# Performance work log

Measured on AMD Instinct MI355X. Metric: run time of the kernel, lower is better.

## Reference

```python
import jax, jax.numpy as jnp
import numpy as np

N = 100000
E = 3200000
D = 128


def setup_inputs() -> dict:
    key = jax.random.key(0)
    k1, k2, k3, k4 = jax.random.split(key, 4)
    x = jax.random.normal(k1, (N, D), dtype=jnp.float32)
    edge_index = jax.random.randint(k2, (2, E), 0, N, dtype=jnp.int64)
    W1 = jax.random.normal(k3, (D, 16), dtype=jnp.float32) * (1.0 / np.sqrt(D))
    b1 = jnp.zeros((16,), dtype=jnp.float32)
    W2 = jax.random.normal(k4, (16, 2), dtype=jnp.float32) * (1.0 / np.sqrt(16))
    b2 = jnp.zeros((2,), dtype=jnp.float32)
    return {"x": x, "edge_index": edge_index, "W1": W1, "b1": b1, "W2": W2, "b2": b2}


def _gcn_conv(h, src, dst, norm, W, b):
    # transform first (out_dim <= in_dim), then normalized scatter-add aggregation
    h = h @ W                                   # [N, out]
    msg = h[src] * norm[:, None]                # [E+N, out] gathered messages
    agg = jax.ops.segment_sum(msg, dst, num_segments=N)
    return agg + b


def reference(x, edge_index, W1, b1, W2, b2):
    loops = jnp.arange(N, dtype=edge_index.dtype)
    src = jnp.concatenate([edge_index[0], loops])   # row (message source)
    dst = jnp.concatenate([edge_index[1], loops])   # col (aggregation target)
    # symmetric GCN normalization: deg over dst, norm = d^-1/2[src] * d^-1/2[dst]
    deg = jax.ops.segment_sum(jnp.ones_like(src, dtype=x.dtype), dst, num_segments=N)
    dinv = jnp.where(deg > 0, jax.lax.rsqrt(deg), 0.0)
    norm = dinv[src] * dinv[dst]

    h = _gcn_conv(x, src, dst, norm, W1, b1)
    h = jax.nn.relu(h)
    h = _gcn_conv(h, src, dst, norm, W2, b2)
    return jax.nn.log_softmax(h, axis=1)
```

## Files before the change

### kernel.cpp

```cpp
#include <hip/hip_runtime.h>
#include <hip/hip_fp16.h>
#include <math.h>

#define N_NODES 100000
#define N_EDGES 3200000
#define D_IN    128
#define H1      16

#define BSH     8
#define NPB     256
#define NB      391
#define CAP     13056
#define PBLK    512
#define CHUNK   6250
#define ELS_CAP 12128
#define NLINES  (ELS_CAP / 16)
#define MROWS   64


__global__ __launch_bounds__(512) void k_zero(int* __restrict__ cursor) {
    int t = threadIdx.x;
    if (t < NB) cursor[t] = 0;
}

__global__ __launch_bounds__(512) void k_partition(const int* __restrict__ ei,
                                                   int* __restrict__ cursor,
                                                   unsigned int* __restrict__ eop) {
    __shared__ int h[512];
    __shared__ int loff[512];
    __shared__ int resv[NB];
    __shared__ unsigned short owner[NLINES];
    __shared__ unsigned char rank8[CHUNK];
    __shared__ unsigned int els[ELS_CAP];
    int t = threadIdx.x;
    h[t] = 0;
    __syncthreads();
    int c0 = blockIdx.x * CHUNK;
    const int* srcs = ei + c0;
    const int* dsts = ei + N_EDGES + c0;
    for (int i = t; i < CHUNK; i += 512)
        rank8[i] = (unsigned char)atomicAdd(&h[dsts[i] >> BSH], 1);
    __syncthreads();
    int cp = (h[t] + 15) & ~15;
    loff[t] = cp;
    __syncthreads();
    for (int o = 1; o < 512; o <<= 1) {
        int u = (t >= o) ? loff[t - o] : 0;
        __syncthreads();
        loff[t] += u;
        __syncthreads();
    }
    int inc = loff[t];
    int totalpad = loff[511];
    int ex = inc - cp;
    __syncthreads();
    loff[t] = ex;
    if (t < NB && cp) {
        resv[t] = atomicAdd(&cursor[t], cp);
        int l0 = ex >> 4;
        for (int k = 0; k < (cp >> 4); ++k) owner[l0 + k] = (unsigned short)t;
    }
    for (int i = t; i < totalpad; i += 512) els[i] = 0xFFFFFFFFu;
    __syncthreads();
    for (int i = t; i < CHUNK; i += 512) {
        int s = srcs[i];
        int d = dsts[i];
        int b = d >> BSH;
        els[loff[b] + (int)rank8[i]] = ((unsigned)s << BSH) | (unsigned)(d & (NPB - 1));
    }
    __syncthreads();
    for (int i = t; i < totalpad; i += 512) {
        int b   = owner[i >> 4];
        int pos = resv[b] + (i - loff[b]);
        if (pos < CAP)
            eop[(size_t)b * CAP + pos] = els[i];
    }
}

__global__ __launch_bounds__(512) void k_build(const int* __restrict__ cursor,
                                               unsigned int* __restrict__ eop,
                                               int* __restrict__ nstart,
                                               int* __restrict__ ndeg,
                                               float* __restrict__ dinv) {
    __shared__ unsigned int els[CAP];
    __shared__ int cnt[NPB];
    __shared__ int off[NPB];
    __shared__ int cur[NPB];
    int t = threadIdx.x, b = blockIdx.x;
    if (t < NPB) cnt[t] = 0;
    __syncthreads();
    int n = cursor[b]; if (n > CAP) n = CAP;
    unsigned int* reg = eop + (size_t)b * CAP;
    for (int i = t; i < n; i += 512) {
        unsigned int v = reg[i];
        els[i] = v;
        if ((int)v >= 0) atomicAdd(&cnt[v & (NPB - 1)], 1);
    }
    __syncthreads();
    int val = (t < NPB) ? cnt[t] : 0;
    if (t < NPB) off[t] = val;
    __syncthreads();
    for (int o = 1; o < NPB; o <<= 1) {
        int u = 0;
        if (t < NPB && t >= o) u = off[t - o];
        __syncthreads();
        if (t < NPB) off[t] += u;
        __syncthreads();
    }
    if (t < NPB) {
        int ex = off[t] - val;
        int node = (b << BSH) + t;
        if (node < N_NODES) {
            nstart[node] = b * CAP + ex;
            ndeg[node]   = val;
            dinv[node]   = rsqrtf((float)(val + 1));
        }
        cur[t] = ex;
    }
    __syncthreads();
    for (int i = t; i < n; i += 512) {
        unsigned int v = els[i];
        if ((int)v >= 0) {
            int r = atomicAdd(&cur[v & (NPB - 1)], 1);
            reg[r] = v >> BSH;
        }
    }
}

__global__ __launch_bounds__(256) void k_mm1(const float* __restrict__ x,
                                             const float* __restrict__ W1,
                                             const float* __restrict__ dinv,
                                             __half* __restrict__ h1h) {
    __shared__ float sX[MROWS][D_IN + 1];
    int t = threadIdx.x;
    int r0 = blockIdx.x * MROWS;
    for (int i = t; i < MROWS * (D_IN / 4); i += 256) {
        int row = i >> 5, c4 = i & 31;
        int grow = r0 + row;
        float4 v = (grow < N_NODES) ? ((const float4*)x)[(size_t)grow * 32 + c4]
                                    : make_float4(0.f, 0.f, 0.f, 0.f);
        sX[row][c4 * 4 + 0] = v.x; sX[row][c4 * 4 + 1] = v.y;
        sX[row][c4 * 4 + 2] = v.z; sX[row][c4 * 4 + 3] = v.w;
    }
    __syncthreads();
    int lane = t & 63;
    int c0 = __builtin_amdgcn_readfirstlane((t >> 6) * 4);
    float a0 = 0.f, a1 = 0.f, a2 = 0.f, a3 = 0.f;
#pragma unroll 4
    for (int d = 0; d < D_IN; ++d) {
        float xv = sX[lane][d];
        a0 = fmaf(xv, W1[d * 16 + c0 + 0], a0);
        a1 = fmaf(xv, W1[d * 16 + c0 + 1], a1);
        a2 = fmaf(xv, W1[d * 16 + c0 + 2], a2);
        a3 = fmaf(xv, W1[d * 16 + c0 + 3], a3);
    }
    int grow = r0 + lane;
    if (grow < N_NODES) {
        float di = dinv[grow];
        __half2* o = (__half2*)(h1h + (size_t)grow * H1 + c0);
        o[0] = __floats2half2_rn(a0 * di, a1 * di);
        o[1] = __floats2half2_rn(a2 * di, a3 * di);
    }
}

__global__ __launch_bounds__(256) void k_agg1(const unsigned int* __restrict__ eop,
                                              const int* __restrict__ nstart,
                                              const int* __restrict__ ndeg,
                                              const __half* __restrict__ h1h,
                                              const float* __restrict__ dinv,
                                              const float* __restrict__ b1,
                                              const float* __restrict__ W2,
                                              float2* __restrict__ h2f) {
    int t = threadIdx.x;
    int g = t >> 4, l = t & 15;
    int node = blockIdx.x * 16 + g;
    int e0 = nstart[node], e1 = e0 + ndeg[node];
    float acc = 0.f;
    int j = e0;
    for (; j + 4 <= e1; j += 4) {
        int s0 = eop[j], s1 = eop[j + 1], s2 = eop[j + 2], s3 = eop[j + 3];
        acc += __half2float(h1h[s0 * H1 + l]) + __half2float(h1h[s1 * H1 + l])
             + __half2float(h1h[s2 * H1 + l]) + __half2float(h1h[s3 * H1 + l]);
    }
    for (; j < e1; ++j) acc += __half2float(h1h[(int)eop[j] * H1 + l]);
    float di = dinv[node];
    float s  = acc + __half2float(h1h[node * H1 + l]);
    float h  = fmaxf(fmaf(di, s, b1[l]), 0.f);
    float p0 = h * W2[2 * l], p1 = h * W2[2 * l + 1];
#pragma unroll
    for (int off = 1; off < 16; off <<= 1) {
        p0 += __shfl_xor(p0, off);
        p1 += __shfl_xor(p1, off);
    }
    if (l == 0) h2f[node] = make_float2(p0 * di, p1 * di);
}

__global__ __launch_bounds__(256) void k_agg2(const unsigned int* __restrict__ eop,
                                              const int* __restrict__ nstart,
                                              const int* __restrict__ ndeg,
                                              const float2* __restrict__ h2f,
                                              const float* __restrict__ dinv,
                                              const float* __restrict__ b2,
                                              float* __restrict__ out) {
    int tg = blockIdx.x * 256 + threadIdx.x;
    int node = tg >> 2, l = tg & 3;
    if (node >= N_NODES) return;
    int e0 = nstart[node], e1 = e0 + ndeg[node];
    float ax = 0.f, ay = 0.f;
    for (int j = e0 + l; j < e1; j += 4) {
        float2 m = h2f[eop[j]];
        ax += m.x; ay += m.y;
    }
    ax += __shfl_xor(ax, 1); ay += __shfl_xor(ay, 1);
    ax += __shfl_xor(ax, 2); ay += __shfl_xor(ay, 2);
    if (l == 0) {
        float di = dinv[node];
        float2 self = h2f[node];
        float a0 = fmaf(di, ax + self.x, b2[0]);
        float a1 = fmaf(di, ay + self.y, b2[1]);
        float m  = fmaxf(a0, a1);
        float lg = logf(expf(a0 - m) + expf(a1 - m));
        out[2 * node]     = a0 - m - lg;
        out[2 * node + 1] = a1 - m - lg;
    }
}

extern "C" void kernel_launch(void* const* d_in, const int* in_sizes, int n_in,
                              void* d_out, int out_size, void* d_ws, size_t ws_size,
                              hipStream_t stream) {
    const float* x  = (const float*)d_in[0];
    const int*   ei = (const int*)d_in[1];
    const float* W1 = (const float*)d_in[2];
    const float* b1 = (const float*)d_in[3];
    const float* W2 = (const float*)d_in[4];
    const float* b2 = (const float*)d_in[5];
    float* out = (float*)d_out;

    int*          cursor = (int*)d_ws;
    int*          nstart = cursor + 512;
    int*          ndeg   = nstart + 100352;
    float*        dinv   = (float*)(ndeg + 100352);
    __half*       h1h    = (__half*)(dinv + 100352);
    float2*       h2f    = (float2*)(h1h + (size_t)100352 * H1);
    unsigned int* eop    = (unsigned int*)(h2f + 100352);

    k_zero     <<<1,    512, 0, stream>>>(cursor);
    k_partition<<<PBLK, 512, 0, stream>>>(ei, cursor, eop);
    k_build    <<<NB,   512, 0, stream>>>(cursor, eop, nstart, ndeg, dinv);
    k_mm1      <<<(N_NODES + MROWS - 1) / MROWS, 256, 0, stream>>>(x, W1, dinv, h1h);
    k_agg1     <<<N_NODES / 16, 256, 0, stream>>>(eop, nstart, ndeg, h1h, dinv, b1, W2, h2f);
    k_agg2     <<<(N_NODES * 4 + 255) / 256, 256, 0, stream>>>(eop, nstart, ndeg, h2f, dinv, b2, out);
}
```

Baseline: 222.0 us.

## Replace per-node CSR build with bucket-local shared-memory atomic aggregation

Drops the in-bucket counting sort that built per-node CSR offsets, keeping only a degree count. Both aggregation kernels now run one block per 256-node bucket, stream the unsorted packed edge list, and accumulate messages with shared-memory float atomics before the epilogue. This removes the prefix scan, the scatter rewrite of the edge array and the nstart/ndeg arrays. In exchange it adds LDS atomic contention, makes summation order nondeterministic, and limits aggregation to 391 blocks, which may lower occupancy.

```diff
diff --git a/kernel.cpp b/kernel.cpp
--- a/kernel.cpp
+++ b/kernel.cpp
@@ -77,53 +77,24 @@
     }
 }
 
-__global__ __launch_bounds__(512) void k_build(const int* __restrict__ cursor,
-                                               unsigned int* __restrict__ eop,
-                                               int* __restrict__ nstart,
-                                               int* __restrict__ ndeg,
-                                               float* __restrict__ dinv) {
-    __shared__ unsigned int els[CAP];
+__global__ __launch_bounds__(512) void k_deg(const int* __restrict__ cursor,
+                                             const unsigned int* __restrict__ eop,
+                                             float* __restrict__ dinv) {
     __shared__ int cnt[NPB];
-    __shared__ int off[NPB];
-    __shared__ int cur[NPB];
     int t = threadIdx.x, b = blockIdx.x;
     if (t < NPB) cnt[t] = 0;
     __syncthreads();
     int n = cursor[b]; if (n > CAP) n = CAP;
-    unsigned int* reg = eop + (size_t)b * CAP;
+    const unsigned int* reg = eop + (size_t)b * CAP;
     for (int i = t; i < n; i += 512) {
         unsigned int v = reg[i];
-        els[i] = v;
         if ((int)v >= 0) atomicAdd(&cnt[v & (NPB - 1)], 1);
     }
     __syncthreads();
-    int val = (t < NPB) ? cnt[t] : 0;
-    if (t < NPB) off[t] = val;
-    __syncthreads();
-    for (int o = 1; o < NPB; o <<= 1) {
-        int u = 0;
-        if (t < NPB && t >= o) u = off[t - o];
-        __syncthreads();
-        if (t < NPB) off[t] += u;
-        __syncthreads();
-    }
     if (t < NPB) {
-        int ex = off[t] - val;
         int node = (b << BSH) + t;
-        if (node < N_NODES) {
-            nstart[node] = b * CAP + ex;
-            ndeg[node]   = val;
-            dinv[node]   = rsqrtf((float)(val + 1));
-        }
-        cur[t] = ex;
-    }
-    __syncthreads();
-    for (int i = t; i < n; i += 512) {
-        unsigned int v = els[i];
-        if ((int)v >= 0) {
-            int r = atomicAdd(&cur[v & (NPB - 1)], 1);
-            reg[r] = v >> BSH;
-        }
+        if (node < N_NODES)
+            dinv[node] = rsqrtf((float)(cnt[t] + 1));
     }
 }
 
@@ -163,65 +134,124 @@
     }
 }
 
-__global__ __launch_bounds__(256) void k_agg1(const unsigned int* __restrict__ eop,
-                                              const int* __restrict__ nstart,
-                                              const int* __restrict__ ndeg,
+__global__ __launch_bounds__(512) void k_agg1(const int* __restrict__ cursor,
+                                              const unsigned int* __restrict__ eop,
                                               const __half* __restrict__ h1h,
                                               const float* __restrict__ dinv,
                                               const float* __restrict__ b1,
                                               const float* __restrict__ W2,
                                               float2* __restrict__ h2f) {
-    int t = threadIdx.x;
+    __shared__ float acc[NPB * H1];
+    int t = threadIdx.x, b = blockIdx.x;
+    for (int i = t; i < NPB * H1; i += 512) acc[i] = 0.f;
+    __syncthreads();
+    int n = cursor[b]; if (n > CAP) n = CAP;
+    const unsigned int* reg = eop + (size_t)b * CAP;
     int g = t >> 4, l = t & 15;
-    int node = blockIdx.x * 16 + g;
-    int e0 = nstart[node], e1 = e0 + ndeg[node];
-    float acc = 0.f;
-    int j = e0;
-    for (; j + 4 <= e1; j += 4) {
-        int s0 = eop[j], s1 = eop[j + 1], s2 = eop[j + 2], s3 = eop[j + 3];
-        acc += __half2float(h1h[s0 * H1 + l]) + __half2float(h1h[s1 * H1 + l])
-             + __half2float(h1h[s2 * H1 + l]) + __half2float(h1h[s3 * H1 + l]);
-    }
-    for (; j < e1; ++j) acc += __half2float(h1h[(int)eop[j] * H1 + l]);
-    float di = dinv[node];
-    float s  = acc + __half2float(h1h[node * H1 + l]);
-    float h  = fmaxf(fmaf(di, s, b1[l]), 0.f);
-    float p0 = h * W2[2 * l], p1 = h * W2[2 * l + 1];
+    int nmain = n & ~127;
+    int i0 = 0;
+    for (; i0 < nmain; i0 += 128) {
+        int idx = i0 + g;
+        unsigned int v0 = reg[idx      ];
+        unsigned int v1 = reg[idx +  32];
+        unsigned int v2 = reg[idx +  64];
+        unsigned int v3 = reg[idx +  96];
+        unsigned s0 = ((int)v0 >= 0) ? (v0 >> BSH) : 0u;
+        unsigned s1 = ((int)v1 >= 0) ? (v1 >> BSH) : 0u;
+        unsigned s2 = ((int)v2 >= 0) ? (v2 >> BSH) : 0u;
+        unsigned s3 = ((int)v3 >= 0) ? (v3 >> BSH) : 0u;
+        float f0 = __half2float(h1h[s0 * H1 + l]);
+        float f1 = __half2float(h1h[s1 * H1 + l]);
+        float f2 = __half2float(h1h[s2 * H1 + l]);
+        float f3 = __half2float(h1h[s3 * H1 + l]);
+        atomicAdd(&acc[(v0 & (NPB - 1)) * H1 + l], ((int)v0 >= 0) ? f0 : 0.f);
+        atomicAdd(&acc[(v1 & (NPB - 1)) * H1 + l], ((int)v1 >= 0) ? f1 : 0.f);
+        atomicAdd(&acc[(v2 & (NPB - 1)) * H1 + l], ((int)v2 >= 0) ? f2 : 0.f);
+        atomicAdd(&acc[(v3 & (NPB - 1)) * H1 + l], ((int)v3 >= 0) ? f3 : 0.f);
+    }
+    for (int i = nmain + g; i < n; i += 32) {
+        unsigned int v = reg[i];
+        unsigned s = ((int)v >= 0) ? (v >> BSH) : 0u;
+        float f = __half2float(h1h[s * H1 + l]);
+        atomicAdd(&acc[(v & (NPB - 1)) * H1 + l], ((int)v >= 0) ? f : 0.f);
+    }
+    __syncthreads();
+    for (int p = 0; p < NPB / 32; ++p) {
+        int nl = p * 32 + g;
+        int node = (b << BSH) + nl;
+        if (node < N_NODES) {
+            float s = acc[nl * H1 + l] + __half2float(h1h[(size_t)node * H1 + l]);
+            float di = dinv[node];
+            float h = fmaxf(fmaf(di, s, b1[l]), 0.f);
+            float p0 = h * W2[2 * l], p1 = h * W2[2 * l + 1];
 #pragma unroll
-    for (int off = 1; off < 16; off <<= 1) {
-        p0 += __shfl_xor(p0, off);
-        p1 += __shfl_xor(p1, off);
-    }
-    if (l == 0) h2f[node] = make_float2(p0 * di, p1 * di);
-}
-
-__global__ __launch_bounds__(256) void k_agg2(const unsigned int* __restrict__ eop,
-                                              const int* __restrict__ nstart,
-                                              const int* __restrict__ ndeg,
+            for (int off = 1; off < 16; off <<= 1) {
+                p0 += __shfl_xor(p0, off);
+                p1 += __shfl_xor(p1, off);
+            }
+            if (l == 0) h2f[node] = make_float2(p0 * di, p1 * di);
+        }
+    }
+}
+
+__global__ __launch_bounds__(512) void k_agg2(const int* __restrict__ cursor,
+                                              const unsigned int* __restrict__ eop,
                                               const float2* __restrict__ h2f,
                                               const float* __restrict__ dinv,
                                               const float* __restrict__ b2,
                                               float* __restrict__ out) {
-    int tg = blockIdx.x * 256 + threadIdx.x;
-    int node = tg >> 2, l = tg & 3;
-    if (node >= N_NODES) return;
-    int e0 = nstart[node], e1 = e0 + ndeg[node];
-    float ax = 0.f, ay = 0.f;
-    for (int j = e0 + l; j < e1; j += 4) {
-        float2 m = h2f[eop[j]];
-        ax += m.x; ay += m.y;
-    }
-    ax += __shfl_xor(ax, 1); ay += __shfl_xor(ay, 1);
-    ax += __shfl_xor(ax, 2); ay += __shfl_xor(ay, 2);
-    if (l == 0) {
-        float di = dinv[node];
-        float2 self = h2f[node];
-        float a0 = fmaf(di, ax + self.x, b2[0]);
-        float a1 = fmaf(di, ay + self.y, b2[1]);
-        float m  = fmaxf(a0, a1);
-        float lg = logf(expf(a0 - m) + expf(a1 - m));
-        out[2 * node]     = a0 - m - lg;
-        out[2 * node + 1] = a1 - m - lg;
+    __shared__ float accx[NPB];
+    __shared__ float accy[NPB];
+    int t = threadIdx.x, b = blockIdx.x;
+    if (t < NPB) { accx[t] = 0.f; accy[t] = 0.f; }
+    __syncthreads();
+    int n = cursor[b]; if (n > CAP) n = CAP;
+    const unsigned int* reg = eop + (size_t)b * CAP;
+    int nmain = n & ~2047;
+    int i0 = 0;
+    for (; i0 < nmain; i0 += 2048) {
+        int idx = i0 + t;
+        unsigned int v0 = reg[idx       ];
+        unsigned int v1 = reg[idx +  512];
+        unsigned int v2 = reg[idx + 1024];
+        unsigned int v3 = reg[idx + 1536];
+        unsigned s0 = ((int)v0 >= 0) ? (v0 >> BSH) : 0u;
+        unsigned s1 = ((int)v1 >= 0) ? (v1 >> BSH) : 0u;
+        unsigned s2 = ((int)v2 >= 0) ? (v2 >> BSH) : 0u;
+        unsigned s3 = ((int)v3 >= 0) ? (v3 >> BSH) : 0u;
+        float2 m0 = h2f[s0];
+        float2 m1 = h2f[s1];
+        float2 m2 = h2f[s2];
+        float2 m3 = h2f[s3];
+        atomicAdd(&accx[v0 & (NPB - 1)], ((int)v0 >= 0) ? m0.x : 0.f);
+        atomicAdd(&accy[v0 & (NPB - 1)], ((int)v0 >= 0) ? m0.y : 0.f);
+        atomicAdd(&accx[v1 & (NPB - 1)], ((int)v1 >= 0) ? m1.x : 0.f);
+        atomicAdd(&accy[v1 & (NPB - 1)], ((int)v1 >= 0) ? m1.y : 0.f);
+        atomicAdd(&accx[v2 & (NPB - 1)], ((int)v2 >= 0) ? m2.x : 0.f);
+        atomicAdd(&accy[v2 & (NPB - 1)], ((int)v2 >= 0) ? m2.y : 0.f);
+        atomicAdd(&accx[v3 & (NPB - 1)], ((int)v3 >= 0) ? m3.x : 0.f);
+        atomicAdd(&accy[v3 & (NPB - 1)], ((int)v3 >= 0) ? m3.y : 0.f);
+    }
+    for (int i = nmain + t; i < n; i += 512) {
+        unsigned int v = reg[i];
+        unsigned s = ((int)v >= 0) ? (v >> BSH) : 0u;
+        float2 m = h2f[s];
+        atomicAdd(&accx[v & (NPB - 1)], ((int)v >= 0) ? m.x : 0.f);
+        atomicAdd(&accy[v & (NPB - 1)], ((int)v >= 0) ? m.y : 0.f);
+    }
+    __syncthreads();
+    if (t < NPB) {
+        int node = (b << BSH) + t;
+        if (node < N_NODES) {
+            float di = dinv[node];
+            float2 self = h2f[node];
+            float a0 = fmaf(di, accx[t] + self.x, b2[0]);
+            float a1 = fmaf(di, accy[t] + self.y, b2[1]);
+            float m  = fmaxf(a0, a1);
+            float lg = logf(expf(a0 - m) + expf(a1 - m));
+            out[2 * node]     = a0 - m - lg;
+            out[2 * node + 1] = a1 - m - lg;
+        }
     }
 }
 
@@ -237,17 +267,15 @@
     float* out = (float*)d_out;
 
     int*          cursor = (int*)d_ws;
-    int*          nstart = cursor + 512;
-    int*          ndeg   = nstart + 100352;
-    float*        dinv   = (float*)(ndeg + 100352);
+    float*        dinv   = (float*)(cursor + 512);
     __half*       h1h    = (__half*)(dinv + 100352);
     float2*       h2f    = (float2*)(h1h + (size_t)100352 * H1);
     unsigned int* eop    = (unsigned int*)(h2f + 100352);
 
     k_zero     <<<1,    512, 0, stream>>>(cursor);
     k_partition<<<PBLK, 512, 0, stream>>>(ei, cursor, eop);
-    k_build    <<<NB,   512, 0, stream>>>(cursor, eop, nstart, ndeg, dinv);
+    k_deg      <<<NB,   512, 0, stream>>>(cursor, eop, dinv);
     k_mm1      <<<(N_NODES + MROWS - 1) / MROWS, 256, 0, stream>>>(x, W1, dinv, h1h);
-    k_agg1     <<<N_NODES / 16, 256, 0, stream>>>(eop, nstart, ndeg, h1h, dinv, b1, W2, h2f);
-    k_agg2     <<<(N_NODES * 4 + 255) / 256, 256, 0, stream>>>(eop, nstart, ndeg, h2f, dinv, b2, out);
-}
+    k_agg1     <<<NB,   512, 0, stream>>>(cursor, eop, h1h, dinv, b1, W2, h2f);
+    k_agg2     <<<NB,   512, 0, stream>>>(cursor, eop, h2f, dinv, b2, out);
+}
```

Measured after the change: 713.2 us. 3.21x slower.
